# Performance work log

Hardware: AMD Instinct MI355X
Metric: run time of the kernel (lower is better)

Reference implementation:

```python
import jax, jax.numpy as jnp
import numpy as np

B, S, H = 1, 1024, 2048
E, I, TOP_K = 64, 768, 8


def setup_inputs() -> dict:
    key = jax.random.key(0)
    k1, k2, k3, k4, k5 = jax.random.split(key, 5)
    std = 0.02
    return {
        "hidden_states": jax.random.normal(k1, (B, S, H), dtype=jnp.float32),
        "router_w": jax.random.normal(k2, (E, H), dtype=jnp.float32) * std,
        "gate_w": jax.random.normal(k3, (E, I, H), dtype=jnp.float32) * std,
        "up_w": jax.random.normal(k4, (E, I, H), dtype=jnp.float32) * std,
        "down_w": jax.random.normal(k5, (E, H, I), dtype=jnp.float32) * std,
    }


def reference(hidden_states, router_w, gate_w, up_w, down_w):
    b, s, h = hidden_states.shape
    x = hidden_states.reshape(-1, h)                     # [T, H]
    T = x.shape[0]

    # Router: softmax in fp32, top-k, renormalize (matches torch source).
    logits = x @ router_w.T                              # [T, E]
    probs = jax.nn.softmax(logits.astype(jnp.float32), axis=-1)
    topk_w, topk_idx = jax.lax.top_k(probs, TOP_K)       # [T, K]
    topk_w = topk_w / jnp.sum(topk_w, axis=-1, keepdims=True)
    topk_w = topk_w.astype(hidden_states.dtype)

    # Dense combine weights: zero for unselected experts. [T, E]
    tok = jnp.arange(T)[:, None]
    combine = jnp.zeros((T, E), dtype=hidden_states.dtype).at[tok, topk_idx].add(topk_w)

    # Scan over experts: SwiGLU MLP on all tokens, weighted-accumulate.
    # Tokens with zero combine weight contribute nothing (same math as the
    # gather/scatter loop in the torch source).
    def body(acc, p):
        gw, uw, dw, cw = p                                # [I,H],[I,H],[H,I],[T]
        hidden = jax.nn.silu(x @ gw.T) * (x @ uw.T)       # [T, I]
        out = hidden @ dw.T                               # [T, H]
        return acc + cw[:, None] * out, None

    init = jnp.zeros_like(x)
    final, _ = jax.lax.scan(body, init, (gate_w, up_w, down_w, combine.T))
    return final.reshape(b, s, h)
```

## Files before the change

kernel.cpp:

```cpp
#include <hip/hip_runtime.h>

#define T_TOK 1024
#define HD    2048
#define NE    64
#define ID    768
#define TOPK  8

typedef __bf16 bf16x8 __attribute__((ext_vector_type(8)));
typedef __bf16 bf16x4 __attribute__((ext_vector_type(4)));
typedef float  f32x4  __attribute__((ext_vector_type(4)));

__device__ __forceinline__ void load_lds16(const void* src, void* lds) {
  __builtin_amdgcn_global_load_lds(
      (const __attribute__((address_space(1))) void*)src,
      (__attribute__((address_space(3))) void*)lds, 16, 0, 0);
}

__global__ __launch_bounds__(256) void router_kernel(
    const float* __restrict__ x, const float* __restrict__ rw,
    unsigned short* __restrict__ xb_u, float* __restrict__ tw,
    int* __restrict__ counts, int* __restrict__ lists)
{
  __shared__ float  sx[HD];
  __shared__ double slog[NE];
  const int t = blockIdx.x;
  const int tid = threadIdx.x;
  __bf16* xb = (__bf16*)xb_u;

  for (int i = tid; i < HD; i += 256) {
    float v = x[(size_t)t * HD + i];
    sx[i] = v;
    xb[(size_t)t * HD + i] = (__bf16)v;
  }
  __syncthreads();

  const int e = tid >> 2, p = tid & 3;
  const float* rwrow = rw + (size_t)e * HD;
  double acc = 0.0;
  for (int k = p; k < HD; k += 4)
    acc += (double)sx[k] * (double)rwrow[k];
  acc += __shfl_xor(acc, 1, 64);
  acc += __shfl_xor(acc, 2, 64);
  if (p == 0) slog[e] = acc;
  __syncthreads();

  if (tid < 64) {
    double v = slog[tid];
    double selv = -1e300; int seli = 0; double gmax = 0.0;
    #pragma unroll
    for (int k = 0; k < TOPK; ++k) {
      double bv = v; int bi = tid;
      #pragma unroll
      for (int off = 32; off >= 1; off >>= 1) {
        double ov = __shfl_xor(bv, off, 64);
        int    oi = __shfl_xor(bi, off, 64);
        if (ov > bv || (ov == bv && oi < bi)) { bv = ov; bi = oi; }
      }
      if (k == 0) gmax = bv;
      if (tid == k) { selv = bv; seli = bi; }
      if (tid == bi) v = -1e300;
    }
    double e_ = (tid < TOPK) ? exp(selv - gmax) : 0.0;
    double s = e_;
    #pragma unroll
    for (int off = 32; off >= 1; off >>= 1) s += __shfl_xor(s, off, 64);
    if (tid < TOPK) {
      int slot = t * TOPK + tid;
      tw[slot] = (float)(e_ / s);
      int pos = atomicAdd(&counts[seli], 1);
      lists[seli * T_TOK + pos] = slot;
    }
  }
}

__global__ __launch_bounds__(512, 4) void gemm1_kernel(
    const unsigned short* __restrict__ xb_u,
    const float* __restrict__ gw, const float* __restrict__ uw,
    const int* __restrict__ counts, const int* __restrict__ lists,
    const unsigned short* __restrict__ zp_u,
    unsigned short* __restrict__ hb_u)
{
  __shared__ __bf16 sA[2][256 * 32];
  __shared__ __bf16 sG[2][64 * 32];
  __shared__ __bf16 sU[2][64 * 32];
  __shared__ int    sSlot[256];

  const __bf16* xb = (const __bf16*)xb_u;
  const __bf16* zp = (const __bf16*)zp_u;
  __bf16* hb = (__bf16*)hb_u;

  const int wg  = blockIdx.x;
  const int idx = wg >> 3;
  const int e   = (wg & 7) * 8 + idx / 12;
  const int n0  = (idx % 12) * 64;

  const int tid  = threadIdx.x;
  const int wid  = tid >> 6;
  const int lane = tid & 63;
  const int n_e  = counts[e];

  const int wrow = tid >> 3;
  const int wqc  = tid & 7;
  const size_t wsrc0 = ((size_t)e * ID + n0 + wrow) * HD + (size_t)wqc * 4;
  const int wds = wrow * 32 + (((wqc >> 1) ^ ((wrow >> 1) & 3)) * 8) + (wqc & 1) * 4;

  for (int m0 = 0; m0 < n_e; m0 += 256) {
    if (tid < 256) sSlot[tid] = (m0 + tid < n_e) ? lists[e * T_TOK + m0 + tid] : -1;
    __syncthreads();

    const __bf16* abase[2];
    #pragma unroll
    for (int j = 0; j < 2; ++j) {
      int r = wid * 32 + j * 16 + (lane >> 2);
      int slot = sSlot[r];
      int cs = (lane & 3) ^ ((r >> 1) & 3);
      abase[j] = (slot >= 0) ? (xb + (size_t)(slot >> 3) * HD + cs * 8)
                             : (zp + cs * 8);
    }

    f32x4 accg[2][4], accu[2][4];
    const f32x4 vzero = {0.f, 0.f, 0.f, 0.f};
    #pragma unroll
    for (int r = 0; r < 2; ++r)
      #pragma unroll
      for (int c = 0; c < 4; ++c) { accg[r][c] = vzero; accu[r][c] = vzero; }

    const int rows_here = n_e - m0 - wid * 32;

    #pragma unroll
    for (int j = 0; j < 2; ++j)
      load_lds16(abase[j], &sA[0][(wid * 32 + j * 16) * 32]);
    f32x4 ga = *(const f32x4*)(gw + wsrc0);
    f32x4 ua = *(const f32x4*)(uw + wsrc0);
    f32x4 gb_, ub_;

#define G1_STEP(KT, BC, BN_, GC, UC, GN, UN)                                      \
    {                                                                             \
      bf16x4 gv, uv;                                                              \
      _Pragma("unroll") for (int q = 0; q < 4; ++q) {                             \
        gv[q] = (__bf16)GC[q]; uv[q] = (__bf16)UC[q];                             \
      }                                                                           \
      *(bf16x4*)&sG[BC][wds] = gv;                                                \
      *(bf16x4*)&sU[BC][wds] = uv;                                                \
      __syncthreads();                                                            \
      if ((KT) + 1 < HD / 32) {                                                   \
        const int k1 = ((KT) + 1) * 32;                                           \
        _Pragma("unroll") for (int j = 0; j < 2; ++j)                             \
          load_lds16(abase[j] + k1, &sA[BN_][(wid * 32 + j * 16) * 32]);          \
        GN = *(const f32x4*)(gw + wsrc0 + (size_t)k1);                            \
        UN = *(const f32x4*)(uw + wsrc0 + (size_t)k1);                            \
      }                                                                           \
      bf16x8 aF[2];                                                               \
      _Pragma("unroll") for (int r = 0; r < 2; ++r) if (r * 16 < rows_here) {     \
        int row = wid * 32 + r * 16 + (lane & 15);                                \
        int ph = (lane >> 4) ^ ((row >> 1) & 3);                                  \
        aF[r] = *(const bf16x8*)&sA[BC][row * 32 + ph * 8];                       \
      }                                                                           \
      _Pragma("unroll") for (int c = 0; c < 4; ++c) {                             \
        int row = c * 16 + (lane & 15);                                           \
        int ph = (lane >> 4) ^ ((row >> 1) & 3);                                  \
        bf16x8 gF = *(const bf16x8*)&sG[BC][row * 32 + ph * 8];                   \
        bf16x8 uF = *(const bf16x8*)&sU[BC][row * 32 + ph * 8];                   \
        _Pragma("unroll") for (int r = 0; r < 2; ++r) if (r * 16 < rows_here) {   \
          accg[r][c] = __builtin_amdgcn_mfma_f32_16x16x32_bf16(aF[r], gF, accg[r][c], 0, 0, 0); \
          accu[r][c] = __builtin_amdgcn_mfma_f32_16x16x32_bf16(aF[r], uF, accu[r][c], 0, 0, 0); \
        }                                                                         \
      }                                                                           \
    }

    for (int it = 0; it < (HD / 32) / 2; ++it) {
      G1_STEP(2 * it,     0, 1, ga,  ua,  gb_, ub_);
      G1_STEP(2 * it + 1, 1, 0, gb_, ub_, ga,  ua);
    }
#undef G1_STEP

    #pragma unroll
    for (int r = 0; r < 2; ++r) if (r * 16 < rows_here) {
      #pragma unroll
      for (int j = 0; j < 4; ++j) {
        int row = wid * 32 + r * 16 + (lane >> 4) * 4 + j;
        if (m0 + row < n_e) {
          int slot = sSlot[row];
          #pragma unroll
          for (int c = 0; c < 4; ++c) {
            float g = accg[r][c][j], u = accu[r][c][j];
            float h = (g / (1.0f + expf(-g))) * u;
            hb[(size_t)slot * ID + (size_t)(n0 + c * 16 + (lane & 15))] = (__bf16)h;
          }
        }
      }
    }
    __syncthreads();
  }
}

__global__ __launch_bounds__(512, 4) void gemm2_kernel(
    const unsigned short* __restrict__ hb_u,
    const float* __restrict__ dw,
    const int* __restrict__ counts, const int* __restrict__ lists,
    const float* __restrict__ tw,
    const unsigned short* __restrict__ zp_u,
    float* __restrict__ out)
{
  __shared__ __bf16 sA[2][256 * 32];
  __shared__ __bf16 sB[2][64 * 32];
  __shared__ int    sSlot[256];

  const __bf16* hbuf = (const __bf16*)hb_u;
  const __bf16* zp   = (const __bf16*)zp_u;

  const int wg  = blockIdx.x;
  const int idx = wg >> 3;
  const int e   = (wg & 7) * 8 + idx / 32;
  const int n0  = (idx % 32) * 64;

  const int tid  = threadIdx.x;
  const int wid  = tid >> 6;
  const int lane = tid & 63;
  const int n_e  = counts[e];

  const int wrow = tid >> 3;
  const int wqc  = tid & 7;
  const size_t wsrc0 = ((size_t)e * HD + n0 + wrow) * ID + (size_t)wqc * 4;
  const int wds = wrow * 32 + (((wqc >> 1) ^ ((wrow >> 1) & 3)) * 8) + (wqc & 1) * 4;

  for (int m0 = 0; m0 < n_e; m0 += 256) {
    if (tid < 256) sSlot[tid] = (m0 + tid < n_e) ? lists[e * T_TOK + m0 + tid] : -1;
    __syncthreads();

    const __bf16* abase[2];
    #pragma unroll
    for (int j = 0; j < 2; ++j) {
      int r = wid * 32 + j * 16 + (lane >> 2);
      int slot = sSlot[r];
      int cs = (lane & 3) ^ ((r >> 1) & 3);
      abase[j] = (slot >= 0) ? (hbuf + (size_t)slot * ID + cs * 8)
                             : (zp + cs * 8);
    }

    f32x4 acc[2][4];
    const f32x4 vzero = {0.f, 0.f, 0.f, 0.f};
    #pragma unroll
    for (int r = 0; r < 2; ++r)
      #pragma unroll
      for (int c = 0; c < 4; ++c) acc[r][c] = vzero;

    const int rows_here = n_e - m0 - wid * 32;

    #pragma unroll
    for (int j = 0; j < 2; ++j)
      load_lds16(abase[j], &sA[0][(wid * 32 + j * 16) * 32]);
    f32x4 da = *(const f32x4*)(dw + wsrc0);
    f32x4 db_;

#define G2_STEP(KT, BC, BN_, DC, DN)                                              \
    {                                                                             \
      bf16x4 dv;                                                                  \
      _Pragma("unroll") for (int q = 0; q < 4; ++q) dv[q] = (__bf16)DC[q];        \
      *(bf16x4*)&sB[BC][wds] = dv;                                                \
      __syncthreads();                                                            \
      if ((KT) + 1 < ID / 32) {                                                   \
        const int k1 = ((KT) + 1) * 32;                                           \
        _Pragma("unroll") for (int j = 0; j < 2; ++j)                             \
          load_lds16(abase[j] + k1, &sA[BN_][(wid * 32 + j * 16) * 32]);          \
        DN = *(const f32x4*)(dw + wsrc0 + (size_t)k1);                            \
      }                                                                           \
      bf16x8 aF[2];                                                               \
      _Pragma("unroll") for (int r = 0; r < 2; ++r) if (r * 16 < rows_here) {     \
        int row = wid * 32 + r * 16 + (lane & 15);                                \
        int ph = (lane >> 4) ^ ((row >> 1) & 3);                                  \
        aF[r] = *(const bf16x8*)&sA[BC][row * 32 + ph * 8];                       \
      }                                                                           \
      _Pragma("unroll") for (int c = 0; c < 4; ++c) {                             \
        int row = c * 16 + (lane & 15);                                           \
        int ph = (lane >> 4) ^ ((row >> 1) & 3);                                  \
        bf16x8 bF = *(const bf16x8*)&sB[BC][row * 32 + ph * 8];                   \
        _Pragma("unroll") for (int r = 0; r < 2; ++r) if (r * 16 < rows_here) {   \
          acc[r][c] = __builtin_amdgcn_mfma_f32_16x16x32_bf16(aF[r], bF, acc[r][c], 0, 0, 0); \
        }                                                                         \
      }                                                                           \
    }

    for (int it = 0; it < (ID / 32) / 2; ++it) {
      G2_STEP(2 * it,     0, 1, da,  db_);
      G2_STEP(2 * it + 1, 1, 0, db_, da);
    }
#undef G2_STEP

    #pragma unroll
    for (int r = 0; r < 2; ++r) if (r * 16 < rows_here) {
      #pragma unroll
      for (int j = 0; j < 4; ++j) {
        int row = wid * 32 + r * 16 + (lane >> 4) * 4 + j;
        if (m0 + row < n_e) {
          int slot = sSlot[row];
          int token = slot >> 3;
          float w = tw[slot];
          #pragma unroll
          for (int c = 0; c < 4; ++c) {
            atomicAdd(out + (size_t)token * HD + (size_t)(n0 + c * 16 + (lane & 15)),
                      w * acc[r][c][j]);
          }
        }
      }
    }
    __syncthreads();
  }
}

extern "C" void kernel_launch(void* const* d_in, const int* in_sizes, int n_in,
                              void* d_out, int out_size, void* d_ws, size_t ws_size,
                              hipStream_t stream) {
  const float* x  = (const float*)d_in[0];
  const float* rw = (const float*)d_in[1];
  const float* gw = (const float*)d_in[2];
  const float* uw = (const float*)d_in[3];
  const float* dw = (const float*)d_in[4];
  float* out = (float*)d_out;

  char* ws = (char*)d_ws;
  const size_t ZP_OFF  = 0;
  const size_t XB_OFF  = 8192;
  const size_t TW_OFF  = XB_OFF + (size_t)T_TOK * HD * 2;
  const size_t CNT_OFF = TW_OFF + (size_t)T_TOK * TOPK * 4;
  const size_t LST_OFF = CNT_OFF + 256;
  const size_t HB_OFF  = LST_OFF + (size_t)NE * T_TOK * 4;

  unsigned short* zp  = (unsigned short*)(ws + ZP_OFF);
  unsigned short* xb  = (unsigned short*)(ws + XB_OFF);
  float*          tw  = (float*)(ws + TW_OFF);
  int*            cnt = (int*)(ws + CNT_OFF);
  int*            lst = (int*)(ws + LST_OFF);
  unsigned short* hb  = (unsigned short*)(ws + HB_OFF);

  hipMemsetAsync(zp, 0, 8192, stream);
  hipMemsetAsync(cnt, 0, 256, stream);
  hipMemsetAsync(d_out, 0, (size_t)T_TOK * HD * sizeof(float), stream);

  router_kernel<<<T_TOK, 256, 0, stream>>>(x, rw, xb, tw, cnt, lst);
  gemm1_kernel<<<768, 512, 0, stream>>>(xb, gw, uw, cnt, lst, zp, hb);
  gemm2_kernel<<<2048, 512, 0, stream>>>(hb, dw, cnt, lst, tw, zp, out);
}
```

Measured before the change: 504.7 us.

## Drop LDS staging in expert GEMMs and stream operands straight into registers

```diff
diff --git a/kernel.cpp b/kernel.cpp
--- a/kernel.cpp
+++ b/kernel.cpp
@@ -7,13 +7,13 @@
 #define TOPK  8
 
 typedef __bf16 bf16x8 __attribute__((ext_vector_type(8)));
-typedef __bf16 bf16x4 __attribute__((ext_vector_type(4)));
 typedef float  f32x4  __attribute__((ext_vector_type(4)));
 
-__device__ __forceinline__ void load_lds16(const void* src, void* lds) {
-  __builtin_amdgcn_global_load_lds(
-      (const __attribute__((address_space(1))) void*)src,
-      (__attribute__((address_space(3))) void*)lds, 16, 0, 0);
+__device__ __forceinline__ bf16x8 cvt8(f32x4 a, f32x4 b) {
+  bf16x8 r;
+  #pragma unroll
+  for (int j = 0; j < 4; ++j) { r[j] = (__bf16)a[j]; r[j + 4] = (__bf16)b[j]; }
+  return r;
 }
 
 __global__ __launch_bounds__(256) void router_kernel(
@@ -73,238 +73,152 @@
   }
 }
 
-__global__ __launch_bounds__(512, 4) void gemm1_kernel(
+__global__ __launch_bounds__(256, 3) void gemm1_kernel(
     const unsigned short* __restrict__ xb_u,
     const float* __restrict__ gw, const float* __restrict__ uw,
     const int* __restrict__ counts, const int* __restrict__ lists,
-    const unsigned short* __restrict__ zp_u,
     unsigned short* __restrict__ hb_u)
 {
-  __shared__ __bf16 sA[2][256 * 32];
-  __shared__ __bf16 sG[2][64 * 32];
-  __shared__ __bf16 sU[2][64 * 32];
-  __shared__ int    sSlot[256];
-
-  const __bf16* xb = (const __bf16*)xb_u;
-  const __bf16* zp = (const __bf16*)zp_u;
+  const char* xbp = (const char*)xb_u;
   __bf16* hb = (__bf16*)hb_u;
 
   const int wg  = blockIdx.x;
   const int idx = wg >> 3;
-  const int e   = (wg & 7) * 8 + idx / 12;
-  const int n0  = (idx % 12) * 64;
-
-  const int tid  = threadIdx.x;
-  const int wid  = tid >> 6;
-  const int lane = tid & 63;
-  const int n_e  = counts[e];
-
-  const int wrow = tid >> 3;
-  const int wqc  = tid & 7;
-  const size_t wsrc0 = ((size_t)e * ID + n0 + wrow) * HD + (size_t)wqc * 4;
-  const int wds = wrow * 32 + (((wqc >> 1) ^ ((wrow >> 1) & 3)) * 8) + (wqc & 1) * 4;
-
-  for (int m0 = 0; m0 < n_e; m0 += 256) {
-    if (tid < 256) sSlot[tid] = (m0 + tid < n_e) ? lists[e * T_TOK + m0 + tid] : -1;
-    __syncthreads();
-
-    const __bf16* abase[2];
-    #pragma unroll
-    for (int j = 0; j < 2; ++j) {
-      int r = wid * 32 + j * 16 + (lane >> 2);
-      int slot = sSlot[r];
-      int cs = (lane & 3) ^ ((r >> 1) & 3);
-      abase[j] = (slot >= 0) ? (xb + (size_t)(slot >> 3) * HD + cs * 8)
-                             : (zp + cs * 8);
-    }
-
-    f32x4 accg[2][4], accu[2][4];
-    const f32x4 vzero = {0.f, 0.f, 0.f, 0.f};
-    #pragma unroll
-    for (int r = 0; r < 2; ++r)
-      #pragma unroll
-      for (int c = 0; c < 4; ++c) { accg[r][c] = vzero; accu[r][c] = vzero; }
-
-    const int rows_here = n_e - m0 - wid * 32;
-
-    #pragma unroll
-    for (int j = 0; j < 2; ++j)
-      load_lds16(abase[j], &sA[0][(wid * 32 + j * 16) * 32]);
-    f32x4 ga = *(const f32x4*)(gw + wsrc0);
-    f32x4 ua = *(const f32x4*)(uw + wsrc0);
-    f32x4 gb_, ub_;
-
-#define G1_STEP(KT, BC, BN_, GC, UC, GN, UN)                                      \
-    {                                                                             \
-      bf16x4 gv, uv;                                                              \
-      _Pragma("unroll") for (int q = 0; q < 4; ++q) {                             \
-        gv[q] = (__bf16)GC[q]; uv[q] = (__bf16)UC[q];                             \
-      }                                                                           \
-      *(bf16x4*)&sG[BC][wds] = gv;                                                \
-      *(bf16x4*)&sU[BC][wds] = uv;                                                \
-      __syncthreads();                                                            \
-      if ((KT) + 1 < HD / 32) {                                                   \
-        const int k1 = ((KT) + 1) * 32;                                           \
-        _Pragma("unroll") for (int j = 0; j < 2; ++j)                             \
-          load_lds16(abase[j] + k1, &sA[BN_][(wid * 32 + j * 16) * 32]);          \
-        GN = *(const f32x4*)(gw + wsrc0 + (size_t)k1);                            \
-        UN = *(const f32x4*)(uw + wsrc0 + (size_t)k1);                            \
-      }                                                                           \
-      bf16x8 aF[2];                                                               \
-      _Pragma("unroll") for (int r = 0; r < 2; ++r) if (r * 16 < rows_here) {     \
-        int row = wid * 32 + r * 16 + (lane & 15);                                \
-        int ph = (lane >> 4) ^ ((row >> 1) & 3);                                  \
-        aF[r] = *(const bf16x8*)&sA[BC][row * 32 + ph * 8];                       \
-      }                                                                           \
-      _Pragma("unroll") for (int c = 0; c < 4; ++c) {                             \
-        int row = c * 16 + (lane & 15);                                           \
-        int ph = (lane >> 4) ^ ((row >> 1) & 3);                                  \
-        bf16x8 gF = *(const bf16x8*)&sG[BC][row * 32 + ph * 8];                   \
-        bf16x8 uF = *(const bf16x8*)&sU[BC][row * 32 + ph * 8];                   \
-        _Pragma("unroll") for (int r = 0; r < 2; ++r) if (r * 16 < rows_here) {   \
-          accg[r][c] = __builtin_amdgcn_mfma_f32_16x16x32_bf16(aF[r], gF, accg[r][c], 0, 0, 0); \
-          accu[r][c] = __builtin_amdgcn_mfma_f32_16x16x32_bf16(aF[r], uF, accu[r][c], 0, 0, 0); \
-        }                                                                         \
-      }                                                                           \
-    }
-
-    for (int it = 0; it < (HD / 32) / 2; ++it) {
-      G1_STEP(2 * it,     0, 1, ga,  ua,  gb_, ub_);
-      G1_STEP(2 * it + 1, 1, 0, gb_, ub_, ga,  ua);
-    }
-#undef G1_STEP
-
-    #pragma unroll
-    for (int r = 0; r < 2; ++r) if (r * 16 < rows_here) {
-      #pragma unroll
-      for (int j = 0; j < 4; ++j) {
-        int row = wid * 32 + r * 16 + (lane >> 4) * 4 + j;
-        if (m0 + row < n_e) {
-          int slot = sSlot[row];
-          #pragma unroll
-          for (int c = 0; c < 4; ++c) {
-            float g = accg[r][c][j], u = accu[r][c][j];
-            float h = (g / (1.0f + expf(-g))) * u;
-            hb[(size_t)slot * ID + (size_t)(n0 + c * 16 + (lane & 15))] = (__bf16)h;
-          }
-        }
+  const int e   = (wg & 7) * 8 + idx / 24;
+  const int n0  = (idx % 24) * 32;
+
+  const int tid = threadIdx.x, w = tid >> 6, lane = tid & 63;
+  const int h = w & 1, cg = w >> 1;
+  const int n_e = counts[e];
+
+  int slot[8]; unsigned aoff[8];
+  #pragma unroll
+  for (int f = 0; f < 8; ++f) {
+    int row = (2 * f + h) * 16 + (lane & 15);
+    slot[f] = (row < n_e) ? lists[e * T_TOK + row] : 0;
+    aoff[f] = (unsigned)((slot[f] >> 3) * (HD * 2)) + ((lane >> 4) * 16);
+  }
+
+  const char* gp = (const char*)(gw + (size_t)e * ID * HD);
+  const char* up = (const char*)(uw + (size_t)e * ID * HD);
+  unsigned woff = (unsigned)((n0 + cg * 16 + (lane & 15)) * (HD * 4)) + ((lane >> 4) * 32);
+
+  f32x4 accg[8], accu[8];
+  const f32x4 vzero = {0.f, 0.f, 0.f, 0.f};
+  #pragma unroll
+  for (int f = 0; f < 8; ++f) { accg[f] = vzero; accu[f] = vzero; }
+
+  f32x4 g0 = *(const f32x4*)(gp + woff), g1 = *(const f32x4*)(gp + woff + 16);
+  f32x4 u0 = *(const f32x4*)(up + woff), u1 = *(const f32x4*)(up + woff + 16);
+  bf16x8 gc = cvt8(g0, g1), uc = cvt8(u0, u1);
+  unsigned wo = woff + 128;
+  unsigned ao = 0;
+
+  #pragma unroll 1
+  for (int t = 0; t < HD / 32; ++t) {
+    f32x4 gn0, gn1, un0, un1;
+    const bool pf = (t < HD / 32 - 1);
+    if (pf) {
+      gn0 = *(const f32x4*)(gp + wo); gn1 = *(const f32x4*)(gp + wo + 16);
+      un0 = *(const f32x4*)(up + wo); un1 = *(const f32x4*)(up + wo + 16);
+      wo += 128;
+    }
+    #pragma unroll
+    for (int f = 0; f < 8; ++f) if ((2 * f + h) * 16 < n_e) {
+      bf16x8 aF = *(const bf16x8*)(xbp + (size_t)(aoff[f] + ao));
+      accg[f] = __builtin_amdgcn_mfma_f32_16x16x32_bf16(aF, gc, accg[f], 0, 0, 0);
+      accu[f] = __builtin_amdgcn_mfma_f32_16x16x32_bf16(aF, uc, accu[f], 0, 0, 0);
+    }
+    ao += 64;
+    if (pf) { gc = cvt8(gn0, gn1); uc = cvt8(un0, un1); }
+  }
+
+  #pragma unroll
+  for (int f = 0; f < 8; ++f) if ((2 * f + h) * 16 < n_e) {
+    #pragma unroll
+    for (int j = 0; j < 4; ++j) {
+      int q = (lane >> 4) * 4 + j;
+      int row = (2 * f + h) * 16 + q;
+      int s = __shfl(slot[f], q, 64);
+      if (row < n_e) {
+        float gv = accg[f][j], uv = accu[f][j];
+        float hv = (gv / (1.0f + expf(-gv))) * uv;
+        hb[(size_t)s * ID + (size_t)(n0 + cg * 16 + (lane & 15))] = (__bf16)hv;
       }
     }
-    __syncthreads();
-  }
-}
-
-__global__ __launch_bounds__(512, 4) void gemm2_kernel(
+  }
+}
+
+__global__ __launch_bounds__(256, 4) void gemm2_kernel(
     const unsigned short* __restrict__ hb_u,
     const float* __restrict__ dw,
     const int* __restrict__ counts, const int* __restrict__ lists,
     const float* __restrict__ tw,
-    const unsigned short* __restrict__ zp_u,
     float* __restrict__ out)
 {
-  __shared__ __bf16 sA[2][256 * 32];
-  __shared__ __bf16 sB[2][64 * 32];
-  __shared__ int    sSlot[256];
-
-  const __bf16* hbuf = (const __bf16*)hb_u;
-  const __bf16* zp   = (const __bf16*)zp_u;
+  const char* hbp = (const char*)hb_u;
 
   const int wg  = blockIdx.x;
   const int idx = wg >> 3;
-  const int e   = (wg & 7) * 8 + idx / 32;
-  const int n0  = (idx % 32) * 64;
-
-  const int tid  = threadIdx.x;
-  const int wid  = tid >> 6;
-  const int lane = tid & 63;
-  const int n_e  = counts[e];
-
-  const int wrow = tid >> 3;
-  const int wqc  = tid & 7;
-  const size_t wsrc0 = ((size_t)e * HD + n0 + wrow) * ID + (size_t)wqc * 4;
-  const int wds = wrow * 32 + (((wqc >> 1) ^ ((wrow >> 1) & 3)) * 8) + (wqc & 1) * 4;
-
-  for (int m0 = 0; m0 < n_e; m0 += 256) {
-    if (tid < 256) sSlot[tid] = (m0 + tid < n_e) ? lists[e * T_TOK + m0 + tid] : -1;
-    __syncthreads();
-
-    const __bf16* abase[2];
-    #pragma unroll
-    for (int j = 0; j < 2; ++j) {
-      int r = wid * 32 + j * 16 + (lane >> 2);
-      int slot = sSlot[r];
-      int cs = (lane & 3) ^ ((r >> 1) & 3);
-      abase[j] = (slot >= 0) ? (hbuf + (size_t)slot * ID + cs * 8)
-                             : (zp + cs * 8);
-    }
-
-    f32x4 acc[2][4];
-    const f32x4 vzero = {0.f, 0.f, 0.f, 0.f};
-    #pragma unroll
-    for (int r = 0; r < 2; ++r)
-      #pragma unroll
-      for (int c = 0; c < 4; ++c) acc[r][c] = vzero;
-
-    const int rows_here = n_e - m0 - wid * 32;
-
-    #pragma unroll
-    for (int j = 0; j < 2; ++j)
-      load_lds16(abase[j], &sA[0][(wid * 32 + j * 16) * 32]);
-    f32x4 da = *(const f32x4*)(dw + wsrc0);
-    f32x4 db_;
-
-#define G2_STEP(KT, BC, BN_, DC, DN)                                              \
-    {                                                                             \
-      bf16x4 dv;                                                                  \
-      _Pragma("unroll") for (int q = 0; q < 4; ++q) dv[q] = (__bf16)DC[q];        \
-      *(bf16x4*)&sB[BC][wds] = dv;                                                \
-      __syncthreads();                                                            \
-      if ((KT) + 1 < ID / 32) {                                                   \
-        const int k1 = ((KT) + 1) * 32;                                           \
-        _Pragma("unroll") for (int j = 0; j < 2; ++j)                             \
-          load_lds16(abase[j] + k1, &sA[BN_][(wid * 32 + j * 16) * 32]);          \
-        DN = *(const f32x4*)(dw + wsrc0 + (size_t)k1);                            \
-      }                                                                           \
-      bf16x8 aF[2];                                                               \
-      _Pragma("unroll") for (int r = 0; r < 2; ++r) if (r * 16 < rows_here) {     \
-        int row = wid * 32 + r * 16 + (lane & 15);                                \
-        int ph = (lane >> 4) ^ ((row >> 1) & 3);                                  \
-        aF[r] = *(const bf16x8*)&sA[BC][row * 32 + ph * 8];                       \
-      }                                                                           \
-      _Pragma("unroll") for (int c = 0; c < 4; ++c) {                             \
-        int row = c * 16 + (lane & 15);                                           \
-        int ph = (lane >> 4) ^ ((row >> 1) & 3);                                  \
-        bf16x8 bF = *(const bf16x8*)&sB[BC][row * 32 + ph * 8];                   \
-        _Pragma("unroll") for (int r = 0; r < 2; ++r) if (r * 16 < rows_here) {   \
-          acc[r][c] = __builtin_amdgcn_mfma_f32_16x16x32_bf16(aF[r], bF, acc[r][c], 0, 0, 0); \
-        }                                                                         \
-      }                                                                           \
-    }
-
-    for (int it = 0; it < (ID / 32) / 2; ++it) {
-      G2_STEP(2 * it,     0, 1, da,  db_);
-      G2_STEP(2 * it + 1, 1, 0, db_, da);
-    }
-#undef G2_STEP
-
-    #pragma unroll
-    for (int r = 0; r < 2; ++r) if (r * 16 < rows_here) {
-      #pragma unroll
-      for (int j = 0; j < 4; ++j) {
-        int row = wid * 32 + r * 16 + (lane >> 4) * 4 + j;
-        if (m0 + row < n_e) {
-          int slot = sSlot[row];
-          int token = slot >> 3;
-          float w = tw[slot];
-          #pragma unroll
-          for (int c = 0; c < 4; ++c) {
-            atomicAdd(out + (size_t)token * HD + (size_t)(n0 + c * 16 + (lane & 15)),
-                      w * acc[r][c][j]);
-          }
-        }
+  const int e   = (wg & 7) * 8 + idx / 64;
+  const int n0  = (idx % 64) * 32;
+
+  const int tid = threadIdx.x, w = tid >> 6, lane = tid & 63;
+  const int h = w & 1, cg = w >> 1;
+  const int n_e = counts[e];
+
+  int slot[8]; unsigned aoff[8];
+  #pragma unroll
+  for (int f = 0; f < 8; ++f) {
+    int row = (2 * f + h) * 16 + (lane & 15);
+    slot[f] = (row < n_e) ? lists[e * T_TOK + row] : 0;
+    aoff[f] = (unsigned)(slot[f] * (ID * 2)) + ((lane >> 4) * 16);
+  }
+
+  const char* wp = (const char*)(dw + (size_t)e * HD * ID);
+  unsigned woff = (unsigned)((n0 + cg * 16 + (lane & 15)) * (ID * 4)) + ((lane >> 4) * 32);
+
+  f32x4 acc[8];
+  const f32x4 vzero = {0.f, 0.f, 0.f, 0.f};
+  #pragma unroll
+  for (int f = 0; f < 8; ++f) acc[f] = vzero;
+
+  f32x4 d0 = *(const f32x4*)(wp + woff), d1 = *(const f32x4*)(wp + woff + 16);
+  bf16x8 dc = cvt8(d0, d1);
+  unsigned wo = woff + 128;
+  unsigned ao = 0;
+
+  #pragma unroll 1
+  for (int t = 0; t < ID / 32; ++t) {
+    f32x4 dn0, dn1;
+    const bool pf = (t < ID / 32 - 1);
+    if (pf) {
+      dn0 = *(const f32x4*)(wp + wo); dn1 = *(const f32x4*)(wp + wo + 16);
+      wo += 128;
+    }
+    #pragma unroll
+    for (int f = 0; f < 8; ++f) if ((2 * f + h) * 16 < n_e) {
+      bf16x8 aF = *(const bf16x8*)(hbp + (size_t)(aoff[f] + ao));
+      acc[f] = __builtin_amdgcn_mfma_f32_16x16x32_bf16(aF, dc, acc[f], 0, 0, 0);
+    }
+    ao += 64;
+    if (pf) dc = cvt8(dn0, dn1);
+  }
+
+  #pragma unroll
+  for (int f = 0; f < 8; ++f) if ((2 * f + h) * 16 < n_e) {
+    #pragma unroll
+    for (int j = 0; j < 4; ++j) {
+      int q = (lane >> 4) * 4 + j;
+      int row = (2 * f + h) * 16 + q;
+      int s = __shfl(slot[f], q, 64);
+      if (row < n_e) {
+        float wv = tw[s];
+        int token = s >> 3;
+        atomicAdd(out + (size_t)token * HD + (size_t)(n0 + cg * 16 + (lane & 15)),
+                  wv * acc[f][j]);
       }
     }
-    __syncthreads();
   }
 }
 
@@ -319,25 +233,22 @@
   float* out = (float*)d_out;
 
   char* ws = (char*)d_ws;
-  const size_t ZP_OFF  = 0;
-  const size_t XB_OFF  = 8192;
+  const size_t XB_OFF  = 0;
   const size_t TW_OFF  = XB_OFF + (size_t)T_TOK * HD * 2;
   const size_t CNT_OFF = TW_OFF + (size_t)T_TOK * TOPK * 4;
   const size_t LST_OFF = CNT_OFF + 256;
   const size_t HB_OFF  = LST_OFF + (size_t)NE * T_TOK * 4;
 
-  unsigned short* zp  = (unsigned short*)(ws + ZP_OFF);
   unsigned short* xb  = (unsigned short*)(ws + XB_OFF);
   float*          tw  = (float*)(ws + TW_OFF);
   int*            cnt = (int*)(ws + CNT_OFF);
   int*            lst = (int*)(ws + LST_OFF);
   unsigned short* hb  = (unsigned short*)(ws + HB_OFF);
 
-  hipMemsetAsync(zp, 0, 8192, stream);
   hipMemsetAsync(cnt, 0, 256, stream);
   hipMemsetAsync(d_out, 0, (size_t)T_TOK * HD * sizeof(float), stream);
 
   router_kernel<<<T_TOK, 256, 0, stream>>>(x, rw, xb, tw, cnt, lst);
-  gemm1_kernel<<<768, 512, 0, stream>>>(xb, gw, uw, cnt, lst, zp, hb);
-  gemm2_kernel<<<2048, 512, 0, stream>>>(hb, dw, cnt, lst, tw, zp, out);
-}
+  gemm1_kernel<<<1536, 256, 0, stream>>>(xb, gw, uw, cnt, lst, hb);
+  gemm2_kernel<<<4096, 256, 0, stream>>>(hb, dw, cnt, lst, tw, out);
+}
```

New measurement: 921.7 us. 82.6% more time.
